# Performance work log

Hardware: AMD Instinct MI355X
Metric: run time of the kernel (lower is better)

The kernel has to match this reference:

```python
import jax, jax.numpy as jnp
import numpy as np

N, E, D, H = 50000, 800000, 64, 64  # nodes, edges, feat dim, hidden dim
EPS = 1e-3  # Keras BatchNormalization default epsilon

def bn(x, g, b, mu, v):
    # inference-mode batch norm with moving statistics
    return (x - mu) * jax.lax.rsqrt(v + EPS) * g + b

def gelu(x):
    return jax.nn.gelu(x, approximate=False)  # tf.nn.gelu default is exact

def setup_inputs() -> dict:
    key = jax.random.key(0)
    ks = jax.random.split(key, 24)
    r = lambda i, shape, s=1.0: (jax.random.normal(ks[i], shape, jnp.float32) * s)
    inp = {
        "node_feats": r(0, (N, D)),
        "edge_feats": r(1, (E, D)),
        "src": jax.random.randint(ks[2], (E,), 0, N, jnp.int32),
        "dst": jax.random.randint(ks[3], (E,), 0, N, jnp.int32),
        # message MLP (BN -> Dense(gelu)) x2, input D
        "m_g1": 1.0 + 0.1 * r(4, (D,)), "m_b1": 0.1 * r(5, (D,)),
        "m_mu1": 0.1 * r(6, (D,)), "m_v1": jnp.ones((D,), jnp.float32),
        "m_W1": r(7, (D, H), 1.0 / np.sqrt(D)), "m_c1": jnp.zeros((H,), jnp.float32),
        "m_g2": 1.0 + 0.1 * r(8, (H,)), "m_b2": 0.1 * r(9, (H,)),
        "m_mu2": 0.1 * r(10, (H,)), "m_v2": jnp.ones((H,), jnp.float32),
        "m_W2": r(11, (H, H), 1.0 / np.sqrt(H)), "m_c2": jnp.zeros((H,), jnp.float32),
        # edge transformer MLP (Dense(gelu)) x2, input D
        "e_W1": r(12, (D, H), 1.0 / np.sqrt(D)), "e_c1": jnp.zeros((H,), jnp.float32),
        "e_W2": r(13, (H, H), 1.0 / np.sqrt(H)), "e_c2": jnp.zeros((H,), jnp.float32),
        # update MLP (BN -> Dense(gelu)) x2, input D+H (concat combination)
        "u_g1": 1.0 + 0.1 * r(14, (D + H,)), "u_b1": 0.1 * r(15, (D + H,)),
        "u_mu1": 0.1 * r(16, (D + H,)), "u_v1": jnp.ones((D + H,), jnp.float32),
        "u_W1": r(17, (D + H, H), 1.0 / np.sqrt(D + H)), "u_c1": jnp.zeros((H,), jnp.float32),
        "u_g2": 1.0 + 0.1 * r(18, (H,)), "u_b2": 0.1 * r(19, (H,)),
        "u_mu2": 0.1 * r(20, (H,)), "u_v2": jnp.ones((H,), jnp.float32),
        "u_W2": r(21, (H, H), 1.0 / np.sqrt(H)), "u_c2": jnp.zeros((H,), jnp.float32),
    }
    return inp

def reference(node_feats, edge_feats,
              m_g1, m_b1, m_mu1, m_v1, m_W1, m_c1,
              m_g2, m_b2, m_mu2, m_v2, m_W2, m_c2,
              e_W1, e_c1, e_W2, e_c2,
              u_g1, u_b1, u_mu1, u_v1, u_W1, u_c1,
              u_g2, u_b2, u_mu2, u_v2, u_W2, u_c2,
              src, dst):
    # gather neighbour representations: [E, D]
    nbr = node_feats[dst]
    # base message MLP: (BN -> Dropout(identity at inference) -> Dense gelu) x2
    h = gelu(bn(nbr, m_g1, m_b1, m_mu1, m_v1) @ m_W1 + m_c1)
    msg = gelu(bn(h, m_g2, m_b2, m_mu2, m_v2) @ m_W2 + m_c2)
    # edge transformer: Dense(gelu) x2, gates the messages elementwise
    er = gelu(edge_feats @ e_W1 + e_c1)
    er = gelu(er @ e_W2 + e_c2)
    msg = msg * er  # [E, H]
    # unsorted_segment_mean over source node indices (empty segments -> 0)
    s = jax.ops.segment_sum(msg, src, num_segments=N)
    cnt = jax.ops.segment_sum(jnp.ones((E, 1), msg.dtype), src, num_segments=N)
    agg = s / jnp.maximum(cnt, 1.0)  # [N, H]
    # combine ('concat') and update MLP
    hcat = jnp.concatenate([node_feats, agg], axis=-1)  # [N, D+H]
    h = gelu(bn(hcat, u_g1, u_b1, u_mu1, u_v1) @ u_W1 + u_c1)
    out = gelu(bn(h, u_g2, u_b2, u_mu2, u_v2) @ u_W2 + u_c2)
    return out  # [N, H]
```

## Files before the change

### kernel.cpp

```cpp
#include <hip/hip_runtime.h>
#include <hip/hip_bf16.h>

#define NN 50000
#define NE 800000

typedef __bf16 bf16_t;
typedef bf16_t bf16x8 __attribute__((ext_vector_type(8)));
typedef float f32x4 __attribute__((ext_vector_type(4)));

__device__ __forceinline__ float gelu_f(float x) {
    float v = x * fmaf(x * x, 0.07135481627f, 1.595769122f);
    float e = __expf(-v);
    return x * __builtin_amdgcn_rcpf(1.0f + e);
}

__device__ void fold_frag(int K, const float* W, const float* g, const float* b,
                          const float* mu, const float* v, const float* c,
                          bf16_t* Wf, float* cb, int tid, float* part) {
    const int n = tid & 63, kc = tid >> 6;
    const int nt = n >> 4, lrow = n & 15, nkc = K >> 5;
    const int kq = K >> 2, k0 = kc * kq, k1 = k0 + kq;
    float acc = 0.f;
    for (int k = k0; k < k1; ++k) {
        float w = W[k * 64 + n];
        float s = 1.0f, o = 0.0f;
        if (g) {
            s = g[k] * __frsqrt_rn(v[k] + 1e-3f);
            o = b[k] - mu[k] * s;
        }
        int idx = ((nt * nkc + (k >> 5)) * 64 + ((k >> 3) & 3) * 16 + lrow) * 8 + (k & 7);
        Wf[idx] = (bf16_t)(w * s);
        acc += o * w;
    }
    part[kc * 64 + n] = acc;
    __syncthreads();
    if (kc == 0) cb[n] = c[n] + part[n] + part[64 + n] + part[128 + n] + part[192 + n];
}

__global__ void fold_kernel(
    const float* mg1, const float* mb1, const float* mmu1, const float* mv1,
    const float* mW1, const float* mc1,
    const float* mg2, const float* mb2, const float* mmu2, const float* mv2,
    const float* mW2, const float* mc2,
    const float* eW1, const float* ec1, const float* eW2, const float* ec2,
    const float* ug1, const float* ub1, const float* umu1, const float* uv1,
    const float* uW1, const float* uc1,
    const float* ug2, const float* ub2, const float* umu2, const float* uv2,
    const float* uW2, const float* uc2,
    bf16_t* wcat, bf16_t* uW1f, bf16_t* uW2f,
    float* cm1, float* cm2, float* ce1, float* ce2, float* cu1, float* cu2)
{
    __shared__ float part[256];
    int t = threadIdx.x;
    switch (blockIdx.x) {
        case 0: fold_frag(64,  mW1, mg1, mb1, mmu1, mv1, mc1, wcat,         cm1, t, part); break;
        case 1: fold_frag(64,  mW2, mg2, mb2, mmu2, mv2, mc2, wcat + 4096,  cm2, t, part); break;
        case 2: fold_frag(64,  eW1, nullptr, nullptr, nullptr, nullptr, ec1, wcat + 8192,  ce1, t, part); break;
        case 3: fold_frag(64,  eW2, nullptr, nullptr, nullptr, nullptr, ec2, wcat + 12288, ce2, t, part); break;
        case 4: fold_frag(128, uW1, ug1, ub1, umu1, uv1, uc1, uW1f, cu1, t, part); break;
        case 5: fold_frag(64,  uW2, ug2, ub2, umu2, uv2, uc2, uW2f, cu2, t, part); break;
    }
}

__global__ void hist_kernel(const int* __restrict__ src, int* __restrict__ cnt) {
    int e = blockIdx.x * 256 + threadIdx.x;
    if (e < NE) atomicAdd(&cnt[src[e]], 1);
}

__global__ void scanA_kernel(const int* __restrict__ cnt, int* __restrict__ part,
                             int* __restrict__ btot) {
    __shared__ int s[256];
    int tid = threadIdx.x;
    int i = blockIdx.x * 256 + tid;
    int v = (i < NN) ? cnt[i] : 0;
    s[tid] = v;
    __syncthreads();
    #pragma unroll
    for (int off = 1; off < 256; off <<= 1) {
        int t = (tid >= off) ? s[tid - off] : 0;
        __syncthreads();
        s[tid] += t;
        __syncthreads();
    }
    if (i < NN) part[i] = s[tid] - v;
    if (tid == 255) btot[blockIdx.x] = s[255];
}

__global__ void scanB_kernel(int* __restrict__ btot, int nblk) {
    __shared__ int s[256];
    int tid = threadIdx.x;
    int v = (tid < nblk) ? btot[tid] : 0;
    s[tid] = v;
    __syncthreads();
    #pragma unroll
    for (int off = 1; off < 256; off <<= 1) {
        int t = (tid >= off) ? s[tid - off] : 0;
        __syncthreads();
        s[tid] += t;
        __syncthreads();
    }
    if (tid < nblk) btot[tid] = s[tid] - v;
}

__global__ void scanC_kernel(const int* __restrict__ part, const int* __restrict__ btot,
                             int* __restrict__ woff) {
    int i = blockIdx.x * 256 + threadIdx.x;
    if (i < NN) woff[i] = part[i] + btot[i >> 8];
}

__global__ void fill_kernel(const int* __restrict__ src, int* __restrict__ woff,
                            int* __restrict__ pos) {
    int e = blockIdx.x * 256 + threadIdx.x;
    if (e < NE) pos[e] = atomicAdd(&woff[src[e]], 1);
}

__device__ __forceinline__ void mk_frag_hilo(const float* row, int quad,
        bf16x8& hi0, bf16x8& lo0, bf16x8& hi1, bf16x8& lo1)
{
    #pragma unroll
    for (int j = 0; j < 8; ++j) {
        float x0 = row[quad * 8 + j];
        float x1 = row[32 + quad * 8 + j];
        bf16_t h0 = (bf16_t)x0, h1 = (bf16_t)x1;
        hi0[j] = h0; lo0[j] = (bf16_t)(x0 - (float)h0);
        hi1[j] = h1; lo1[j] = (bf16_t)(x1 - (float)h1);
    }
}

__device__ __forceinline__ bf16x8 ldb(const bf16_t* wf, int slot, int lane) {
    return *(const bf16x8*)(wf + (slot * 64 + lane) * 8);
}

__device__ __forceinline__ void gemm64_hilo(const bf16_t* wf, int m,
        bf16x8 h0, bf16x8 l0, bf16x8 h1, bf16x8 l1, f32x4 (&acc)[4], int lane)
{
    #pragma unroll
    for (int nt = 0; nt < 4; ++nt) {
        bf16x8 b0 = ldb(wf, m * 8 + nt * 2 + 0, lane);
        bf16x8 b1 = ldb(wf, m * 8 + nt * 2 + 1, lane);
        f32x4 c = {0.f, 0.f, 0.f, 0.f};
        c = __builtin_amdgcn_mfma_f32_16x16x32_bf16(h0, b0, c, 0, 0, 0);
        c = __builtin_amdgcn_mfma_f32_16x16x32_bf16(l0, b0, c, 0, 0, 0);
        c = __builtin_amdgcn_mfma_f32_16x16x32_bf16(h1, b1, c, 0, 0, 0);
        c = __builtin_amdgcn_mfma_f32_16x16x32_bf16(l1, b1, c, 0, 0, 0);
        acc[nt] = c;
    }
}

__device__ __forceinline__ void gemm64(const bf16_t* wf, int m,
        bf16x8 a0, bf16x8 a1, f32x4 (&acc)[4], int lane)
{
    #pragma unroll
    for (int nt = 0; nt < 4; ++nt) {
        bf16x8 b0 = ldb(wf, m * 8 + nt * 2 + 0, lane);
        bf16x8 b1 = ldb(wf, m * 8 + nt * 2 + 1, lane);
        f32x4 c = {0.f, 0.f, 0.f, 0.f};
        c = __builtin_amdgcn_mfma_f32_16x16x32_bf16(a0, b0, c, 0, 0, 0);
        c = __builtin_amdgcn_mfma_f32_16x16x32_bf16(a1, b1, c, 0, 0, 0);
        acc[nt] = c;
    }
}

__device__ __forceinline__ void epi_to_frag(const f32x4 (&acc)[4], const float* bias,
        bf16_t* h, int lrow, int quad)
{
    #pragma unroll
    for (int nt = 0; nt < 4; ++nt) {
        float bb = bias[nt * 16 + lrow];
        #pragma unroll
        for (int r = 0; r < 4; ++r)
            h[((nt * 2 + (lrow >> 3)) * 16 + quad * 4 + r) * 8 + (lrow & 7)] =
                (bf16_t)gelu_f(acc[nt][r] + bb);
    }
}

__global__ __launch_bounds__(256) void node_msg_kernel(
    const float* __restrict__ node_feats, const bf16_t* __restrict__ wcat,
    const float* __restrict__ cm1, const float* __restrict__ cm2,
    bf16_t* __restrict__ msg)
{
    __shared__ bf16_t wf[8192];
    __shared__ bf16_t hf[4][1024];

    const int tid  = threadIdx.x;
    const int wave = tid >> 6;
    const int lane = tid & 63;
    const int quad = lane >> 4;
    const int lrow = lane & 15;

    #pragma unroll
    for (int i = 0; i < 4; ++i) {
        int chunk = tid + i * 256;
        *(bf16x8*)(wf + chunk * 8) = *(const bf16x8*)(wcat + chunk * 8);
    }
    __syncthreads();

    const int nbase = blockIdx.x * 64 + wave * 16;
    int arow = nbase + lrow;
    arow = arow < NN ? arow : NN - 1;

    f32x4 acc[4];
    {
        const float* nrow = node_feats + (size_t)arow * 64;
        bf16x8 h0, l0, h1, l1;
        mk_frag_hilo(nrow, quad, h0, l0, h1, l1);
        gemm64_hilo(wf, 0, h0, l0, h1, l1, acc, lane);
        epi_to_frag(acc, cm1, hf[wave], lrow, quad);
    }
    bf16x8 a0 = *(const bf16x8*)(hf[wave] + lane * 8);
    bf16x8 a1 = *(const bf16x8*)(hf[wave] + (lane + 64) * 8);
    gemm64(wf, 1, a0, a1, acc, lane);

    #pragma unroll
    for (int nt = 0; nt < 4; ++nt) {
        float bb = cm2[nt * 16 + lrow];
        #pragma unroll
        for (int r = 0; r < 4; ++r) {
            int row = nbase + quad * 4 + r;
            if (row < NN)
                msg[(size_t)row * 64 + nt * 16 + lrow] = (bf16_t)gelu_f(acc[nt][r] + bb);
        }
    }
}

__global__ __launch_bounds__(256) void edge_kernel(
    const float* __restrict__ edge_feats,
    const int* __restrict__ src, const int* __restrict__ dst,
    const int* __restrict__ pos,
    const bf16_t* __restrict__ wcat,
    const float* __restrict__ ce1, const float* __restrict__ ce2,
    const bf16_t* __restrict__ msg,
    float* __restrict__ s_acc, bf16_t* __restrict__ buf, int use_csr)
{
    __shared__ bf16_t wf[8192];
    __shared__ bf16_t hf[4][1024];

    const int tid  = threadIdx.x;
    const int wave = tid >> 6;
    const int lane = tid & 63;
    const int quad = lane >> 4;
    const int lrow = lane & 15;

    #pragma unroll
    for (int i = 0; i < 4; ++i) {
        int chunk = tid + i * 256;
        *(bf16x8*)(wf + chunk * 8) = *(const bf16x8*)(wcat + 8192 + chunk * 8);
    }
    __syncthreads();

    const int ebase = blockIdx.x * 64 + wave * 16;
    bf16_t* h = hf[wave];

    int erow_id[4];
    #pragma unroll
    for (int r = 0; r < 4; ++r) erow_id[r] = ebase + quad * 4 + r;
    bf16_t mg[4][4];
    #pragma unroll
    for (int r = 0; r < 4; ++r) {
        const bf16_t* mrow = msg + (size_t)dst[erow_id[r]] * 64;
        #pragma unroll
        for (int nt = 0; nt < 4; ++nt) mg[r][nt] = mrow[nt * 16 + lrow];
    }

    f32x4 acc[4];
    {
        const float* efr = edge_feats + (size_t)(ebase + lrow) * 64;
        bf16x8 h0, l0, h1, l1;
        mk_frag_hilo(efr, quad, h0, l0, h1, l1);
        gemm64_hilo(wf, 0, h0, l0, h1, l1, acc, lane);
        epi_to_frag(acc, ce1, h, lrow, quad);
    }
    bf16x8 a0 = *(const bf16x8*)(h + lane * 8);
    bf16x8 a1 = *(const bf16x8*)(h + (lane + 64) * 8);
    gemm64(wf, 1, a0, a1, acc, lane);

    if (use_csr) {
        int pe[4];
        #pragma unroll
        for (int r = 0; r < 4; ++r) pe[r] = pos[erow_id[r]];
        #pragma unroll
        for (int nt = 0; nt < 4; ++nt) {
            float bb = ce2[nt * 16 + lrow];
            #pragma unroll
            for (int r = 0; r < 4; ++r) {
                float er = gelu_f(acc[nt][r] + bb);
                buf[(size_t)pe[r] * 64 + nt * 16 + lrow] = (bf16_t)(er * (float)mg[r][nt]);
            }
        }
    } else {
        #pragma unroll
        for (int nt = 0; nt < 4; ++nt) {
            float bb = ce2[nt * 16 + lrow];
            #pragma unroll
            for (int r = 0; r < 4; ++r) {
                float er = gelu_f(acc[nt][r] + bb);
                unsafeAtomicAdd(&s_acc[(size_t)src[erow_id[r]] * 64 + nt * 16 + lrow],
                                er * (float)mg[r][nt]);
            }
        }
    }
}

__global__ __launch_bounds__(256) void agg_kernel(
    const bf16_t* __restrict__ buf, const int* __restrict__ woff,
    const int* __restrict__ cnt, float* __restrict__ agg)
{
    const int wave = threadIdx.x >> 6;
    const int lane = threadIdx.x & 63;
    const int n = blockIdx.x * 4 + wave;
    const int deg = cnt[n];
    const int end = woff[n];
    const int start = end - deg;

    float s0 = 0.f, s1 = 0.f, s2 = 0.f, s3 = 0.f;
    const bf16_t* p = buf + (size_t)start * 64 + lane;
    int j = start;
    for (; j + 4 <= end; j += 4) {
        s0 += (float)p[0];
        s1 += (float)p[64];
        s2 += (float)p[128];
        s3 += (float)p[192];
        p += 256;
    }
    for (; j < end; ++j) { s0 += (float)p[0]; p += 64; }

    float r = (deg > 0) ? (s0 + s1 + s2 + s3) * __builtin_amdgcn_rcpf((float)deg) : 0.f;
    agg[(size_t)n * 64 + lane] = r;
}

__global__ __launch_bounds__(256) void update_kernel(
    const float* __restrict__ node_feats,
    const float* __restrict__ aggv, const int* __restrict__ cnt,
    const bf16_t* __restrict__ uW1f, const float* __restrict__ cu1,
    const bf16_t* __restrict__ uW2f, const float* __restrict__ cu2,
    float* __restrict__ out)
{
    __shared__ bf16_t w1f[8192];
    __shared__ bf16_t w2f[4096];
    __shared__ bf16_t hf[4][1024];

    const int tid  = threadIdx.x;
    const int wave = tid >> 6;
    const int lane = tid & 63;
    const int quad = lane >> 4;
    const int lrow = lane & 15;

    #pragma unroll
    for (int i = 0; i < 4; ++i) {
        int chunk = tid + i * 256;
        *(bf16x8*)(w1f + chunk * 8) = *(const bf16x8*)(uW1f + chunk * 8);
    }
    #pragma unroll
    for (int i = 0; i < 2; ++i) {
        int chunk = tid + i * 256;
        *(bf16x8*)(w2f + chunk * 8) = *(const bf16x8*)(uW2f + chunk * 8);
    }
    __syncthreads();

    const int nbase = blockIdx.x * 64 + wave * 16;
    int arow = nbase + lrow;
    arow = arow < NN ? arow : NN - 1;

    const float* nf   = node_feats + (size_t)arow * 64;
    const float* srow = aggv + (size_t)arow * 64;
    float inv = cnt ? 1.0f / fmaxf((float)cnt[arow], 1.0f) : 1.0f;

    bf16x8 ah[4], al[4];
    #pragma unroll
    for (int j = 0; j < 8; ++j) {
        float x0 = nf[quad * 8 + j];
        float x1 = nf[32 + quad * 8 + j];
        float x2 = srow[quad * 8 + j] * inv;
        float x3 = srow[32 + quad * 8 + j] * inv;
        bf16_t h0 = (bf16_t)x0, h1 = (bf16_t)x1, h2 = (bf16_t)x2, h3 = (bf16_t)x3;
        ah[0][j] = h0; al[0][j] = (bf16_t)(x0 - (float)h0);
        ah[1][j] = h1; al[1][j] = (bf16_t)(x1 - (float)h1);
        ah[2][j] = h2; al[2][j] = (bf16_t)(x2 - (float)h2);
        ah[3][j] = h3; al[3][j] = (bf16_t)(x3 - (float)h3);
    }

    f32x4 acc[4];
    #pragma unroll
    for (int nt = 0; nt < 4; ++nt) {
        f32x4 c = {0.f, 0.f, 0.f, 0.f};
        #pragma unroll
        for (int kk = 0; kk < 4; ++kk) {
            bf16x8 b = *(const bf16x8*)(w1f + ((nt * 4 + kk) * 64 + lane) * 8);
            c = __builtin_amdgcn_mfma_f32_16x16x32_bf16(ah[kk], b, c, 0, 0, 0);
            c = __builtin_amdgcn_mfma_f32_16x16x32_bf16(al[kk], b, c, 0, 0, 0);
        }
        acc[nt] = c;
    }
    bf16_t* hb = hf[wave];
    epi_to_frag(acc, cu1, hb, lrow, quad);

    bf16x8 ha0 = *(const bf16x8*)(hb + lane * 8);
    bf16x8 ha1 = *(const bf16x8*)(hb + (lane + 64) * 8);
    gemm64(w2f, 0, ha0, ha1, acc, lane);

    #pragma unroll
    for (int nt = 0; nt < 4; ++nt) {
        int col = nt * 16 + lrow;
        float bb = cu2[col];
        #pragma unroll
        for (int r = 0; r < 4; ++r) {
            int row = nbase + quad * 4 + r;
            if (row < NN)
                out[(size_t)row * 64 + col] = gelu_f(acc[nt][r] + bb);
        }
    }
}

extern "C" void kernel_launch(void* const* d_in, const int* in_sizes, int n_in,
                              void* d_out, int out_size, void* d_ws, size_t ws_size,
                              hipStream_t stream) {
    const float* node_feats = (const float*)d_in[0];
    const float* edge_feats = (const float*)d_in[1];
    const int*   src        = (const int*)d_in[2];
    const int*   dst        = (const int*)d_in[3];

    char* ws = (char*)d_ws;
    const bool csr = ws_size >= (size_t)116500000;

    size_t off = 0;
    bf16_t* buf = nullptr; float* agg = nullptr; int* pos = nullptr; bf16_t* msg = nullptr;
    float* s_acc = nullptr; int* cnt = nullptr; int* woff = nullptr;
    int* part = nullptr; int* btot = nullptr;

    if (csr) {
        buf = (bf16_t*)(ws + off); off += (size_t)NE * 128;
        char* aggbase = ws + off;
        agg = (float*)aggbase;     off += (size_t)NN * 256;
        pos = (int*)aggbase;
        msg = (bf16_t*)(aggbase + (size_t)NE * 4);
        cnt  = (int*)(ws + off); off += (size_t)NN * 4;
        woff = (int*)(ws + off); off += (size_t)NN * 4;
        part = (int*)(ws + off); off += (size_t)NN * 4;
        btot = (int*)(ws + off); off += 1024;
    } else {
        s_acc = (float*)(ws + off);  off += (size_t)NN * 256;
        cnt   = (int*)(ws + off);    off += (size_t)NN * 4;
        msg   = (bf16_t*)(ws + off); off += (size_t)NN * 128;
    }
    bf16_t* wcat = (bf16_t*)(ws + off); off += 32768;
    bf16_t* uW1f = (bf16_t*)(ws + off); off += 16384;
    bf16_t* uW2f = (bf16_t*)(ws + off); off += 8192;
    float* cm1 = (float*)(ws + off); off += 256;
    float* cm2 = (float*)(ws + off); off += 256;
    float* ce1 = (float*)(ws + off); off += 256;
    float* ce2 = (float*)(ws + off); off += 256;
    float* cu1 = (float*)(ws + off); off += 256;
    float* cu2 = (float*)(ws + off); off += 256;

    if (csr) {
        hipMemsetAsync(cnt, 0, (size_t)NN * 4, stream);
    } else {
        hipMemsetAsync(s_acc, 0, (size_t)NN * 256 + (size_t)NN * 4, stream);
    }

    fold_kernel<<<6, 256, 0, stream>>>(
        (const float*)d_in[4],  (const float*)d_in[5],  (const float*)d_in[6],  (const float*)d_in[7],
        (const float*)d_in[8],  (const float*)d_in[9],
        (const float*)d_in[10], (const float*)d_in[11], (const float*)d_in[12], (const float*)d_in[13],
        (const float*)d_in[14], (const float*)d_in[15],
        (const float*)d_in[16], (const float*)d_in[17], (const float*)d_in[18], (const float*)d_in[19],
        (const float*)d_in[20], (const float*)d_in[21], (const float*)d_in[22], (const float*)d_in[23],
        (const float*)d_in[24], (const float*)d_in[25],
        (const float*)d_in[26], (const float*)d_in[27], (const float*)d_in[28], (const float*)d_in[29],
        (const float*)d_in[30], (const float*)d_in[31],
        wcat, uW1f, uW2f, cm1, cm2, ce1, ce2, cu1, cu2);

    node_msg_kernel<<<(NN + 63) / 64, 256, 0, stream>>>(node_feats, wcat, cm1, cm2, msg);

    hist_kernel<<<(NE + 255) / 256, 256, 0, stream>>>(src, cnt);

    if (csr) {
        const int NBLK = (NN + 255) / 256;
        scanA_kernel<<<NBLK, 256, 0, stream>>>(cnt, part, btot);
        scanB_kernel<<<1, 256, 0, stream>>>(btot, NBLK);
        scanC_kernel<<<NBLK, 256, 0, stream>>>(part, btot, woff);
        fill_kernel<<<(NE + 255) / 256, 256, 0, stream>>>(src, woff, pos);
    }

    edge_kernel<<<NE / 64, 256, 0, stream>>>(
        edge_feats, src, dst, pos, wcat, ce1, ce2, msg, s_acc, buf, csr ? 1 : 0);

    if (csr) {
        agg_kernel<<<NN / 4, 256, 0, stream>>>(buf, woff, cnt, agg);
        update_kernel<<<(NN + 63) / 64, 256, 0, stream>>>(
            node_feats, agg, nullptr, uW1f, cu1, uW2f, cu2, (float*)d_out);
    } else {
        update_kernel<<<(NN + 63) / 64, 256, 0, stream>>>(
            node_feats, s_acc, cnt, uW1f, cu1, uW2f, cu2, (float*)d_out);
    }
}
```

Before: 518.6 us.

## Fuse CSR slot assignment into edge kernel and stage messages through LDS

Measured after the change: 484.2 us. 6.6% less time.

```diff
diff --git a/kernel.cpp b/kernel.cpp
--- a/kernel.cpp
+++ b/kernel.cpp
@@ -108,12 +108,6 @@
     if (i < NN) woff[i] = part[i] + btot[i >> 8];
 }
 
-__global__ void fill_kernel(const int* __restrict__ src, int* __restrict__ woff,
-                            int* __restrict__ pos) {
-    int e = blockIdx.x * 256 + threadIdx.x;
-    if (e < NE) pos[e] = atomicAdd(&woff[src[e]], 1);
-}
-
 __device__ __forceinline__ void mk_frag_hilo(const float* row, int quad,
         bf16x8& hi0, bf16x8& lo0, bf16x8& hi1, bf16x8& lo1)
 {
@@ -226,14 +220,15 @@
 __global__ __launch_bounds__(256) void edge_kernel(
     const float* __restrict__ edge_feats,
     const int* __restrict__ src, const int* __restrict__ dst,
-    const int* __restrict__ pos,
     const bf16_t* __restrict__ wcat,
     const float* __restrict__ ce1, const float* __restrict__ ce2,
     const bf16_t* __restrict__ msg,
-    float* __restrict__ s_acc, bf16_t* __restrict__ buf, int use_csr)
+    float* __restrict__ s_acc, int* __restrict__ woff,
+    bf16_t* __restrict__ buf, int use_csr)
 {
     __shared__ bf16_t wf[8192];
     __shared__ bf16_t hf[4][1024];
+    __shared__ bf16_t sme[4][1024];
 
     const int tid  = threadIdx.x;
     const int wave = tid >> 6;
@@ -249,53 +244,69 @@
     __syncthreads();
 
     const int ebase = blockIdx.x * 64 + wave * 16;
-    bf16_t* h = hf[wave];
-
-    int erow_id[4];
-    #pragma unroll
-    for (int r = 0; r < 4; ++r) erow_id[r] = ebase + quad * 4 + r;
-    bf16_t mg[4][4];
-    #pragma unroll
-    for (int r = 0; r < 4; ++r) {
-        const bf16_t* mrow = msg + (size_t)dst[erow_id[r]] * 64;
-        #pragma unroll
-        for (int nt = 0; nt < 4; ++nt) mg[r][nt] = mrow[nt * 16 + lrow];
-    }
+    bf16_t* h  = hf[wave];
+    bf16_t* sm = sme[wave];
+    const int r0 = lane >> 3;
+    const int c0 = lane & 7;
+    const int r1 = 8 + r0;
+    const int b0 = r0 * 64 + ((c0 * 8) ^ (((r0 >> 2) & 3) << 4));
+    const int b1 = r1 * 64 + ((c0 * 8) ^ (((r1 >> 2) & 3) << 4));
+
+    int dA = dst[ebase + r0];
+    int dB = dst[ebase + r1];
+    bf16x8 mA = *(const bf16x8*)(msg + (size_t)dA * 64 + c0 * 8);
+    bf16x8 mB = *(const bf16x8*)(msg + (size_t)dB * 64 + c0 * 8);
+    int pe_l = 0;
+    if (use_csr && lane < 16) pe_l = atomicAdd(&woff[src[ebase + lane]], 1);
 
     f32x4 acc[4];
     {
         const float* efr = edge_feats + (size_t)(ebase + lrow) * 64;
-        bf16x8 h0, l0, h1, l1;
-        mk_frag_hilo(efr, quad, h0, l0, h1, l1);
-        gemm64_hilo(wf, 0, h0, l0, h1, l1, acc, lane);
+        bf16x8 h0_, l0_, h1_, l1_;
+        mk_frag_hilo(efr, quad, h0_, l0_, h1_, l1_);
+        gemm64_hilo(wf, 0, h0_, l0_, h1_, l1_, acc, lane);
         epi_to_frag(acc, ce1, h, lrow, quad);
     }
+
+    *(bf16x8*)(sm + b0) = mA;
+    *(bf16x8*)(sm + b1) = mB;
+    __builtin_amdgcn_wave_barrier();
+
     bf16x8 a0 = *(const bf16x8*)(h + lane * 8);
     bf16x8 a1 = *(const bf16x8*)(h + (lane + 64) * 8);
     gemm64(wf, 1, a0, a1, acc, lane);
+    __builtin_amdgcn_wave_barrier();
 
     if (use_csr) {
-        int pe[4];
-        #pragma unroll
-        for (int r = 0; r < 4; ++r) pe[r] = pos[erow_id[r]];
         #pragma unroll
         for (int nt = 0; nt < 4; ++nt) {
             float bb = ce2[nt * 16 + lrow];
             #pragma unroll
             for (int r = 0; r < 4; ++r) {
+                int e = quad * 4 + r;
+                int ci = e * 64 + ((nt * 16 + lrow) ^ (((e >> 2) & 3) << 4));
                 float er = gelu_f(acc[nt][r] + bb);
-                buf[(size_t)pe[r] * 64 + nt * 16 + lrow] = (bf16_t)(er * (float)mg[r][nt]);
+                sm[ci] = (bf16_t)(er * (float)sm[ci]);
             }
         }
+        __builtin_amdgcn_wave_barrier();
+        int peA = __shfl(pe_l, r0);
+        int peB = __shfl(pe_l, r1);
+        bf16x8 gA = *(const bf16x8*)(sm + b0);
+        bf16x8 gB = *(const bf16x8*)(sm + b1);
+        *(bf16x8*)(buf + (size_t)peA * 64 + c0 * 8) = gA;
+        *(bf16x8*)(buf + (size_t)peB * 64 + c0 * 8) = gB;
     } else {
         #pragma unroll
         for (int nt = 0; nt < 4; ++nt) {
             float bb = ce2[nt * 16 + lrow];
             #pragma unroll
             for (int r = 0; r < 4; ++r) {
+                int e = quad * 4 + r;
+                int ci = e * 64 + ((nt * 16 + lrow) ^ (((e >> 2) & 3) << 4));
                 float er = gelu_f(acc[nt][r] + bb);
-                unsafeAtomicAdd(&s_acc[(size_t)src[erow_id[r]] * 64 + nt * 16 + lrow],
-                                er * (float)mg[r][nt]);
+                unsafeAtomicAdd(&s_acc[(size_t)src[ebase + e] * 64 + nt * 16 + lrow],
+                                er * (float)sm[ci]);
             }
         }
     }
@@ -423,7 +434,7 @@
     const bool csr = ws_size >= (size_t)116500000;
 
     size_t off = 0;
-    bf16_t* buf = nullptr; float* agg = nullptr; int* pos = nullptr; bf16_t* msg = nullptr;
+    bf16_t* buf = nullptr; float* agg = nullptr; bf16_t* msg = nullptr;
     float* s_acc = nullptr; int* cnt = nullptr; int* woff = nullptr;
     int* part = nullptr; int* btot = nullptr;
 
@@ -431,7 +442,6 @@
         buf = (bf16_t*)(ws + off); off += (size_t)NE * 128;
         char* aggbase = ws + off;
         agg = (float*)aggbase;     off += (size_t)NN * 256;
-        pos = (int*)aggbase;
         msg = (bf16_t*)(aggbase + (size_t)NE * 4);
         cnt  = (int*)(ws + off); off += (size_t)NN * 4;
         woff = (int*)(ws + off); off += (size_t)NN * 4;
@@ -479,11 +489,10 @@
         scanA_kernel<<<NBLK, 256, 0, stream>>>(cnt, part, btot);
         scanB_kernel<<<1, 256, 0, stream>>>(btot, NBLK);
         scanC_kernel<<<NBLK, 256, 0, stream>>>(part, btot, woff);
-        fill_kernel<<<(NE + 255) / 256, 256, 0, stream>>>(src, woff, pos);
     }
 
     edge_kernel<<<NE / 64, 256, 0, stream>>>(
-        edge_feats, src, dst, pos, wcat, ce1, ce2, msg, s_acc, buf, csr ? 1 : 0);
+        edge_feats, src, dst, wcat, ce1, ce2, msg, s_acc, woff, buf, csr ? 1 : 0);
 
     if (csr) {
         agg_kernel<<<NN / 4, 256, 0, stream>>>(buf, woff, cnt, agg);
```
